# Performance work log

Measured on AMD Instinct MI355X. Metric: run time of the kernel, lower is better.

Reference implementation:

```python
import jax, jax.numpy as jnp
import numpy as np

B, S, D, H = 2, 2048, 2048, 16
HD = D // H  # 128


def setup_inputs() -> dict:
    key = jax.random.key(0)
    ks = jax.random.split(key, 6)
    sc = 0.02
    return {
        "x": jax.random.normal(ks[0], (B, S, D), jnp.float32),
        "attention_mask": jnp.ones((B, S), jnp.int32),
        "w_qkv": jax.random.normal(ks[1], (D, 3 * D), jnp.float32) * sc,
        "b_qkv": jnp.zeros((3 * D,), jnp.float32),
        "w_o": jax.random.normal(ks[2], (D, D), jnp.float32) * sc,
        "b_o": jnp.zeros((D,), jnp.float32),
        "ln1_w": jnp.ones((D,), jnp.float32),
        "w1": jax.random.normal(ks[3], (D, 8 * D), jnp.float32) * sc,
        "b1": jnp.zeros((8 * D,), jnp.float32),
        "w2": jax.random.normal(ks[4], (4 * D, D), jnp.float32) * sc,
        "b2": jnp.zeros((D,), jnp.float32),
        "ln2_w": jnp.ones((D,), jnp.float32),
    }


def rmsnorm(x, w, eps=1e-6):
    rms = jnp.sqrt(jnp.mean(x * x, axis=-1, keepdims=True) + eps)
    return w * (x / rms)


def rope_tables(seq_len, dim, base=10000.0):
    inv_freq = 1.0 / (base ** (jnp.arange(0, dim, 2, dtype=jnp.float32) / dim))
    t = jnp.arange(seq_len, dtype=jnp.float32)
    freqs = t[:, None] * inv_freq[None, :]          # [S, dim/2]
    emb = jnp.concatenate([freqs, freqs], axis=-1)  # [S, dim]
    return jnp.cos(emb), jnp.sin(emb)


def apply_rope(x, cos, sin):
    # Faithful to source: rotate pairs, then out = rot*cos + roll(rot,1)*sin
    xr = x.reshape(*x.shape[:-1], -1, 2)
    x1, x2 = xr[..., 0], xr[..., 1]
    rot = jnp.stack([-x2, x1], axis=-1).reshape(x.shape)
    return rot * cos + jnp.roll(rot, shift=1, axis=-1) * sin


def transformer_layer(x, attention_mask, w_qkv, b_qkv, w_o, b_o, ln1_w, w1, b1, w2, b2, ln2_w):
    residual = x
    qkv = x @ w_qkv + b_qkv                         # [B,S,3D]
    q, k, v = jnp.split(qkv, 3, axis=-1)
    split = lambda t: t.reshape(B, S, H, HD).transpose(0, 2, 1, 3)  # [B,H,S,HD]
    q, k, v = split(q), split(k), split(v)

    cos, sin = rope_tables(S, HD)                   # [S,HD], broadcasts over B,H
    q = apply_rope(q, cos, sin)
    k = apply_rope(k, cos, sin)

    scores = jnp.einsum("bhqd,bhkd->bhqk", q, k) / jnp.sqrt(jnp.float32(HD))
    mask = (attention_mask == 1)[:, None, None, :]  # [B,1,1,S]
    scores = jnp.where(mask, scores, -jnp.inf)
    attn = jax.nn.softmax(scores, axis=-1)
    out = jnp.einsum("bhqk,bhkd->bhqd", attn, v)
    out = out.transpose(0, 2, 1, 3).reshape(B, S, D)
    out = out @ w_o + b_o

    x = rmsnorm(out + residual, ln1_w)
    residual = x
    h = x @ w1 + b1                                 # [B,S,8D]
    h, gate = jnp.split(h, 2, axis=-1)
    h = h * jax.nn.gelu(gate, approximate=False)
    h = h @ w2 + b2
    return rmsnorm(h + residual, ln2_w)


def reference(x, attention_mask, w_qkv, b_qkv, w_o, b_o, ln1_w, w1, b1, w2, b2, ln2_w):
    return transformer_layer(x, attention_mask, w_qkv, b_qkv, w_o, b_o, ln1_w, w1, b1, w2, b2, ln2_w)
```

## Files before the change

### kernel.cpp

```cpp
#include <hip/hip_runtime.h>
#include <cstdint>

typedef unsigned short u16;
typedef __attribute__((ext_vector_type(8))) short short8;
typedef __attribute__((ext_vector_type(8))) unsigned short ushortx8;
typedef __attribute__((ext_vector_type(4))) float floatx4;

#define DEV __device__ __forceinline__

DEV u16 f2bf(float f) {
  union { float f; uint32_t u; } x; x.f = f;
  uint32_t r = x.u + 0x7fffu + ((x.u >> 16) & 1u);
  return (u16)(r >> 16);
}
DEV float bf2f(u16 h) {
  union { float f; uint32_t u; } x; x.u = ((uint32_t)h) << 16;
  return x.f;
}
DEV void gload_lds16(const void* g, void* lds) {
  __builtin_amdgcn_global_load_lds(
      (const __attribute__((address_space(1))) char*)(uintptr_t)g,
      (__attribute__((address_space(3))) char*)(uintptr_t)lds, 16, 0, 0);
}


__global__ __launch_bounds__(256) void k_cvt_bf16(const float* __restrict__ in,
                                                  u16* __restrict__ out, int n) {
  int i = (blockIdx.x * 256 + threadIdx.x) * 4;
  if (i + 3 < n) {
    float4 v = *(const float4*)(in + i);
    ushort4 o;
    o.x = f2bf(v.x); o.y = f2bf(v.y); o.z = f2bf(v.z); o.w = f2bf(v.w);
    *(ushort4*)(out + i) = o;
  }
}

__global__ __launch_bounds__(256) void k_transpose_cvt(const float* __restrict__ W,
                                                       u16* __restrict__ Wt, int R, int C) {
  __shared__ u16 t[32][33];
  int tx = threadIdx.x & 31, ty = threadIdx.x >> 5;
  int r0 = blockIdx.y * 32, c0 = blockIdx.x * 32;
#pragma unroll
  for (int i = ty; i < 32; i += 8)
    t[i][tx] = f2bf(W[(size_t)(r0 + i) * C + c0 + tx]);
  __syncthreads();
#pragma unroll
  for (int i = ty; i < 32; i += 8)
    Wt[(size_t)(c0 + i) * R + r0 + tx] = t[tx][i];
}

__global__ __launch_bounds__(256) void k_rope_tab(float* __restrict__ ct, float* __restrict__ st) {
  int i = blockIdx.x * 256 + threadIdx.x;
  int s = i >> 6, j = i & 63;
  float invf = 1.0f / powf(10000.0f, (float)j * (1.0f / 64.0f));
  float ang = (float)s * invf;
  ct[i] = cosf(ang);
  st[i] = sinf(ang);
}

__global__ __launch_bounds__(256) void k_rope_split(const u16* __restrict__ qkv,
                                                    const float* __restrict__ ct,
                                                    const float* __restrict__ st,
                                                    u16* __restrict__ qr, u16* __restrict__ kr) {
  int bs = blockIdx.x;
  int b = bs >> 11, s = bs & 2047;
  __shared__ float q[2048], k[2048];
  const u16* row = qkv + (size_t)bs * 6144;
  for (int i = threadIdx.x * 4; i < 2048; i += 1024) {
    ushort4 qa = *(const ushort4*)(row + i);
    ushort4 ka = *(const ushort4*)(row + 2048 + i);
    q[i] = bf2f(qa.x); q[i + 1] = bf2f(qa.y); q[i + 2] = bf2f(qa.z); q[i + 3] = bf2f(qa.w);
    k[i] = bf2f(ka.x); k[i + 1] = bf2f(ka.y); k[i + 2] = bf2f(ka.z); k[i + 3] = bf2f(ka.w);
  }
  __syncthreads();
  int i0 = threadIdx.x * 8;
  int h = i0 >> 7, d0 = i0 & 127;
  const float* qh = q + (h << 7);
  const float* kh = k + (h << 7);
  ushortx8 qo, ko;
#pragma unroll
  for (int e = 0; e < 8; ++e) {
    int d = d0 + e;
    int dm1 = (d + 127) & 127;
    float c = ct[(s << 6) + (d & 63)];
    float sn = st[(s << 6) + (d & 63)];
    float rq  = (d & 1)   ? qh[d - 1]   : -qh[d + 1];
    float rq1 = (dm1 & 1) ? qh[dm1 - 1] : -qh[dm1 + 1];
    float rk  = (d & 1)   ? kh[d - 1]   : -kh[d + 1];
    float rk1 = (dm1 & 1) ? kh[dm1 - 1] : -kh[dm1 + 1];
    qo[e] = f2bf(rq * c + rq1 * sn);
    ko[e] = f2bf(rk * c + rk1 * sn);
  }
  size_t obase = (((size_t)b * 16 + h) * 2048 + s) * 128 + d0;
  *(ushortx8*)(qr + obase) = qo;
  *(ushortx8*)(kr + obase) = ko;
}

__global__ __launch_bounds__(256) void k_v_transpose(const u16* __restrict__ qkv,
                                                     u16* __restrict__ vt) {
  __shared__ u16 t[32][33];
  int tx = threadIdx.x & 31, ty = threadIdx.x >> 5;
  int s0 = blockIdx.x * 32;
  int dm0 = (blockIdx.y & 63) * 32;
  int b = blockIdx.y >> 6;
#pragma unroll
  for (int i = ty; i < 32; i += 8)
    t[i][tx] = qkv[((size_t)(b * 2048) + s0 + i) * 6144 + 4096 + dm0 + tx];
  __syncthreads();
#pragma unroll
  for (int i = ty; i < 32; i += 8)
    vt[((size_t)b * 2048 + dm0 + i) * 2048 + s0 + tx] = t[tx][i];
}

template <int EPI>
__global__ __launch_bounds__(512, 2) void k_gemm256(const u16* __restrict__ A,
                                                    const u16* __restrict__ Bt,
                                                    void* __restrict__ C,
                                                    const float* __restrict__ bias,
                                                    int M, int N, int K, int nsplit) {
  __shared__ __align__(16) u16 lds[4][2][8192];
  const int tid = threadIdx.x;
  const int w = tid >> 6, lane = tid & 63;
  const int l15 = lane & 15, l4 = lane >> 4;
  const int wm = w >> 2, wn = w & 3;
  const int nbn = N >> 8;

  const int nwg = gridDim.x;
  const int q = nwg >> 3, r8 = nwg & 7;
  const int xcd = blockIdx.x & 7, loc = blockIdx.x >> 3;
  const int swz = (xcd < r8 ? xcd * (q + 1) : r8 * (q + 1) + (xcd - r8) * q) + loc;
  const int ntiles = nwg / nsplit;
  const int split = swz / ntiles, tix = swz % ntiles;
  const int bm = tix / nbn, bn = tix % nbn;
  const int klen = K / nsplit;
  const int kofs = split * klen;

  const size_t abase = (size_t)bm * 256 * K + kofs;
  const size_t bbase = (size_t)bn * 256 * K + kofs;
  const int nt = klen >> 5;

  const int sr = tid >> 2;
  const int sc = (tid & 3) ^ ((sr >> 1) & 3);
  auto stage = [&](int kt, int li, int op) {
    const u16* src = op ? (Bt + bbase) : (A + abase);
    gload_lds16(src + (size_t)(li * 128 + sr) * K + kt * 32 + sc * 8,
                (void*)&lds[kt & 3][op][(li * 512 + w * 64) * 8]);
  };

  const int fro = l15 * 32 + (l4 ^ ((l15 >> 1) & 3)) * 8;

  floatx4 acc[8][4];
  floatx4 zero = {0.f, 0.f, 0.f, 0.f};
#pragma unroll
  for (int m = 0; m < 8; ++m)
#pragma unroll
    for (int n = 0; n < 4; ++n) acc[m][n] = zero;

  for (int kt = 0; kt < 3; ++kt)
    if (kt < nt) {
      stage(kt, 0, 0); stage(kt, 0, 1);
      stage(kt, 1, 0); stage(kt, 1, 1);
    }

  for (int t = 0; t < nt; ++t) {
    const int buf = t & 3;
    if (t < nt - 2)       asm volatile("s_waitcnt vmcnt(8)" ::: "memory");
    else if (t == nt - 2) asm volatile("s_waitcnt vmcnt(4)" ::: "memory");
    else                  asm volatile("s_waitcnt vmcnt(0)" ::: "memory");
    __builtin_amdgcn_s_barrier();
    asm volatile("" ::: "memory");
    if (t + 3 < nt) {
      stage(t + 3, 0, 0); stage(t + 3, 0, 1);
      stage(t + 3, 1, 0); stage(t + 3, 1, 1);
    }
    const u16* Ab = &lds[buf][0][wm * 4096 + fro];
    const u16* Bb = &lds[buf][1][wn * 2048 + fro];
    short8 av[8], bv[4];
#pragma unroll
    for (int n = 0; n < 4; ++n) bv[n] = *(const short8*)(Bb + n * 512);
#pragma unroll
    for (int i = 0; i < 8; ++i) av[i] = *(const short8*)(Ab + i * 512);
#pragma unroll
    for (int i = 0; i < 8; ++i)
#pragma unroll
      for (int n = 0; n < 4; ++n)
        acc[i][n] = __builtin_amdgcn_mfma_f32_16x16x32_bf16(av[i], bv[n], acc[i][n], 0, 0, 0);
    asm volatile("s_waitcnt lgkmcnt(0)" ::: "memory");
  }

  const int row0 = bm * 256 + wm * 128, col0 = bn * 256 + wn * 64;
  if (EPI == 2) {
    float* P = (float*)C + (size_t)split * M * N;
#pragma unroll
    for (int n = 0; n < 4; ++n) {
      int col = col0 + n * 16 + l15;
#pragma unroll
      for (int m = 0; m < 8; ++m)
#pragma unroll
        for (int j = 0; j < 4; ++j) {
          int row = row0 + m * 16 + l4 * 4 + j;
          P[(size_t)row * N + col] = acc[m][n][j];
        }
    }
  } else {
    __syncthreads();
    u16* ep = ((u16*)lds) + w * 8192;
#pragma unroll
    for (int n = 0; n < 4; ++n) {
      float bb = bias[col0 + n * 16 + l15];
#pragma unroll
      for (int m = 0; m < 8; ++m)
#pragma unroll
        for (int j = 0; j < 4; ++j)
          ep[(m * 16 + l4 * 4 + j) * 64 + n * 16 + l15] = f2bf(acc[m][n][j] + bb);
    }
    const int rr = lane >> 3, cg = lane & 7;
    u16* Cg = (u16*)C;
#pragma unroll
    for (int pass = 0; pass < 16; ++pass) {
      short8 v = *(const short8*)&ep[(pass * 8 + rr) * 64 + cg * 8];
      size_t grow = row0 + pass * 8 + rr;
      *(short8*)&Cg[grow * N + col0 + cg * 8] = v;
    }
  }
}

__global__ __launch_bounds__(512, 4) void k_attn(const u16* __restrict__ Qr,
                                                 const u16* __restrict__ Kr,
                                                 const u16* __restrict__ Vt,
                                                 const int* __restrict__ mask,
                                                 u16* __restrict__ O) {
  constexpr int S = 2048, HD = 128, H = 16;
  __shared__ __align__(16) u16 Ksh[64 * 128];
  __shared__ __align__(16) u16 Vsh[128 * 64];
  __shared__ __align__(16) u16 Psh[8][16 * 72];
  __shared__ float Msh[2048];

  const int bid = blockIdx.x;
  const int xcd = bid & 7, local = bid >> 3;
  const int bh = xcd * 4 + (local >> 4);
  const int qt = local & 15;
  const int b = bh >> 4, h = bh & 15;
  const int tid = threadIdx.x, wave = tid >> 6, lane = tid & 63;
  const int l15 = lane & 15, l4 = lane >> 4;
  const size_t bhs = (size_t)(b * H + h);
  const u16* Qb = Qr + bhs * S * HD;
  const u16* Kb = Kr + bhs * S * HD;
  const u16* Vb = Vt + bhs * HD * S;

  for (int i = tid; i < 2048; i += 512)
    Msh[i] = (mask[b * S + i] == 1) ? 0.0f : -1e30f;

  const int qrow = qt * 128 + wave * 16 + l15;
  short8 qf[4];
#pragma unroll
  for (int kk = 0; kk < 4; ++kk)
    qf[kk] = *(const short8*)&Qb[(size_t)qrow * HD + kk * 32 + l4 * 8];

  float m_run[4], l_run[4];
  floatx4 o_acc[8];
  floatx4 zero = {0.f, 0.f, 0.f, 0.f};
#pragma unroll
  for (int j = 0; j < 4; ++j) { m_run[j] = -1e30f; l_run[j] = 0.f; }
#pragma unroll
  for (int n = 0; n < 8; ++n) o_acc[n] = zero;

  for (int ktile = 0; ktile < S / 64; ++ktile) {
    __syncthreads();
#pragma unroll
    for (int it = 0; it < 2; ++it) {
      int gi = it * 512 + tid;
      {
        int row = gi >> 4, g = gi & 15;
        int gs = (g & 8) | ((g ^ row) & 7);
        gload_lds16(Kb + (size_t)(ktile * 64 + row) * HD + gs * 8,
                    (char*)&Ksh[it * 4096 + wave * 512]);
      }
      {
        int row = gi >> 3, g = gi & 7;
        int gs = (g ^ row) & 7;
        gload_lds16(Vb + (size_t)row * S + ktile * 64 + gs * 8,
                    (char*)&Vsh[it * 4096 + wave * 512]);
      }
    }
    __syncthreads();

    floatx4 s_acc[4];
#pragma unroll
    for (int nf = 0; nf < 4; ++nf) s_acc[nf] = zero;
#pragma unroll
    for (int kk = 0; kk < 4; ++kk) {
#pragma unroll
      for (int nf = 0; nf < 4; ++nf) {
        int key = nf * 16 + l15;
        int G = kk * 4 + l4;
        int lg = (G & 8) | ((G ^ key) & 7);
        short8 kv = *(const short8*)&Ksh[key * 128 + lg * 8];
        s_acc[nf] = __builtin_amdgcn_mfma_f32_16x16x32_bf16(qf[kk], kv, s_acc[nf], 0, 0, 0);
      }
    }

    const float scale = 0.08838834764831845f;
    float p[4][4];
#pragma unroll
    for (int nf = 0; nf < 4; ++nf) {
      float ma = Msh[ktile * 64 + nf * 16 + l15];
#pragma unroll
      for (int j = 0; j < 4; ++j) p[nf][j] = s_acc[nf][j] * scale + ma;
    }
#pragma unroll
    for (int j = 0; j < 4; ++j) {
      float mx = fmaxf(fmaxf(p[0][j], p[1][j]), fmaxf(p[2][j], p[3][j]));
      mx = fmaxf(mx, __shfl_xor(mx, 1));
      mx = fmaxf(mx, __shfl_xor(mx, 2));
      mx = fmaxf(mx, __shfl_xor(mx, 4));
      mx = fmaxf(mx, __shfl_xor(mx, 8));
      float mnew = fmaxf(m_run[j], mx);
      float corr = __expf(m_run[j] - mnew);
      float ps = 0.f;
#pragma unroll
      for (int nf = 0; nf < 4; ++nf) {
        p[nf][j] = __expf(p[nf][j] - mnew);
        ps += p[nf][j];
      }
      ps += __shfl_xor(ps, 1); ps += __shfl_xor(ps, 2);
      ps += __shfl_xor(ps, 4); ps += __shfl_xor(ps, 8);
      l_run[j] = l_run[j] * corr + ps;
      m_run[j] = mnew;
#pragma unroll
      for (int n = 0; n < 8; ++n) o_acc[n][j] *= corr;
    }

#pragma unroll
    for (int nf = 0; nf < 4; ++nf)
#pragma unroll
      for (int j = 0; j < 4; ++j)
        Psh[wave][(l4 * 4 + j) * 72 + nf * 16 + l15] = f2bf(p[nf][j]);

#pragma unroll
    for (int ks = 0; ks < 2; ++ks) {
      short8 pa = *(const short8*)&Psh[wave][l15 * 72 + ks * 32 + l4 * 8];
#pragma unroll
      for (int nf2 = 0; nf2 < 8; ++nf2) {
        int hd = nf2 * 16 + l15;
        int G = ks * 4 + l4;
        short8 vv = *(const short8*)&Vsh[hd * 64 + ((G ^ hd) & 7) * 8];
        o_acc[nf2] = __builtin_amdgcn_mfma_f32_16x16x32_bf16(pa, vv, o_acc[nf2], 0, 0, 0);
      }
    }
  }

#pragma unroll
  for (int j = 0; j < 4; ++j) {
    float inv = 1.0f / l_run[j];
    int srow = qt * 128 + wave * 16 + l4 * 4 + j;
    size_t orow = ((size_t)b * S + srow) * 2048 + h * 128;
#pragma unroll
    for (int nf2 = 0; nf2 < 8; ++nf2)
      O[orow + nf2 * 16 + l15] = f2bf(o_acc[nf2][j] * inv);
  }
}

template <int OUTMODE>
__global__ __launch_bounds__(256) void k_rms_fuse(const float* __restrict__ p0,
                                                  const float* __restrict__ p1,
                                                  const float* __restrict__ bias,
                                                  const float* __restrict__ resid,
                                                  const float* __restrict__ w,
                                                  u16* __restrict__ ob,
                                                  float* __restrict__ of) {
  int row = blockIdx.x;
  int t = threadIdx.x;
  size_t base = (size_t)row * 2048 + t * 8;
  float4 a0 = *(const float4*)(p0 + base);
  float4 a1 = *(const float4*)(p0 + base + 4);
  float4 b0 = *(const float4*)(p1 + base);
  float4 b1 = *(const float4*)(p1 + base + 4);
  float4 r0 = *(const float4*)(resid + base);
  float4 r1 = *(const float4*)(resid + base + 4);
  float4 c0 = *(const float4*)(bias + t * 8);
  float4 c1 = *(const float4*)(bias + t * 8 + 4);
  float v[8];
  v[0] = a0.x + b0.x + r0.x + c0.x; v[1] = a0.y + b0.y + r0.y + c0.y;
  v[2] = a0.z + b0.z + r0.z + c0.z; v[3] = a0.w + b0.w + r0.w + c0.w;
  v[4] = a1.x + b1.x + r1.x + c1.x; v[5] = a1.y + b1.y + r1.y + c1.y;
  v[6] = a1.z + b1.z + r1.z + c1.z; v[7] = a1.w + b1.w + r1.w + c1.w;
  float ss = 0.f;
#pragma unroll
  for (int e = 0; e < 8; ++e) ss += v[e] * v[e];
#pragma unroll
  for (int d = 1; d < 64; d <<= 1) ss += __shfl_xor(ss, d);
  __shared__ float sred[4];
  if ((t & 63) == 0) sred[t >> 6] = ss;
  __syncthreads();
  float tot = sred[0] + sred[1] + sred[2] + sred[3];
  float scale = rsqrtf(tot * (1.0f / 2048.0f) + 1e-6f);
  const float* wp = w + t * 8;
  float o[8];
#pragma unroll
  for (int e = 0; e < 8; ++e) o[e] = v[e] * wp[e] * scale;
  if (OUTMODE == 1) {
    ushort4 q0, q1;
    q0.x = f2bf(o[0]); q0.y = f2bf(o[1]); q0.z = f2bf(o[2]); q0.w = f2bf(o[3]);
    q1.x = f2bf(o[4]); q1.y = f2bf(o[5]); q1.z = f2bf(o[6]); q1.w = f2bf(o[7]);
    *(ushort4*)(ob + base) = q0;
    *(ushort4*)(ob + base + 4) = q1;
  }
  {
    float4 f0, f1;
    f0.x = o[0]; f0.y = o[1]; f0.z = o[2]; f0.w = o[3];
    f1.x = o[4]; f1.y = o[5]; f1.z = o[6]; f1.w = o[7];
    *(float4*)(of + base) = f0;
    *(float4*)(of + base + 4) = f1;
  }
}

__global__ __launch_bounds__(256) void k_gelu_mul(const u16* __restrict__ h,
                                                  u16* __restrict__ act) {
  int i = blockIdx.x * 256 + threadIdx.x;
  int row = i >> 10, c8 = (i & 1023) << 3;
  const u16* hr = h + (size_t)row * 16384 + c8;
  ushortx8 a = *(const ushortx8*)hr;
  ushortx8 g = *(const ushortx8*)(hr + 8192);
  ushortx8 o;
#pragma unroll
  for (int e = 0; e < 8; ++e) {
    float av = bf2f(a[e]), gv = bf2f(g[e]);
    float ge = 0.5f * gv * (1.0f + erff(gv * 0.7071067811865476f));
    o[e] = f2bf(av * ge);
  }
  *(ushortx8*)(act + (size_t)row * 8192 + c8) = o;
}

extern "C" void kernel_launch(void* const* d_in, const int* in_sizes, int n_in,
                              void* d_out, int out_size, void* d_ws, size_t ws_size,
                              hipStream_t stream) {
  const float* x     = (const float*)d_in[0];
  const int*   amask = (const int*)d_in[1];
  const float* w_qkv = (const float*)d_in[2];
  const float* b_qkv = (const float*)d_in[3];
  const float* w_o   = (const float*)d_in[4];
  const float* b_o   = (const float*)d_in[5];
  const float* ln1_w = (const float*)d_in[6];
  const float* w1    = (const float*)d_in[7];
  const float* b1    = (const float*)d_in[8];
  const float* w2    = (const float*)d_in[9];
  const float* b2    = (const float*)d_in[10];
  const float* ln2_w = (const float*)d_in[11];
  float* out = (float*)d_out;

  char* ws = (char*)d_ws;
  u16*   xb    = (u16*)(ws + 0);
  u16*   wqkvT = (u16*)(ws + 16777216);
  u16*   woT   = (u16*)(ws + 41943040);
  u16*   w1T   = (u16*)(ws + 50331648);
  u16*   w2T   = (u16*)(ws + 117440512);
  float* ctab  = (float*)(ws + 150994944);
  float* stab  = (float*)(ws + 151519232);
  u16*   qkv   = (u16*)(ws + 152043520);
  u16*   qr    = (u16*)(ws + 202375168);
  u16*   kr    = (u16*)(ws + 219152384);
  u16*   vt    = (u16*)(ws + 235929600);
  u16*   aout  = (u16*)(ws + 252706816);
  u16*   x1b   = (u16*)(ws + 303038464);
  float* x1f   = (float*)(ws + 319815680);
  float* p01   = (float*)(ws + 152043520);
  u16*   hbuf  = (u16*)(ws + 152043520);
  u16*   act   = (u16*)(ws + 0);

  k_cvt_bf16<<<8192, 256, 0, stream>>>(x, xb, 4096 * 2048);
  k_transpose_cvt<<<dim3(192, 64), 256, 0, stream>>>(w_qkv, wqkvT, 2048, 6144);
  k_transpose_cvt<<<dim3(64, 64), 256, 0, stream>>>(w_o, woT, 2048, 2048);
  k_transpose_cvt<<<dim3(512, 64), 256, 0, stream>>>(w1, w1T, 2048, 16384);
  k_transpose_cvt<<<dim3(64, 256), 256, 0, stream>>>(w2, w2T, 8192, 2048);
  k_rope_tab<<<512, 256, 0, stream>>>(ctab, stab);

  k_gemm256<0><<<16 * 24, 512, 0, stream>>>(xb, wqkvT, qkv, b_qkv, 4096, 6144, 2048, 1);
  k_rope_split<<<4096, 256, 0, stream>>>(qkv, ctab, stab, qr, kr);
  k_v_transpose<<<dim3(64, 128), 256, 0, stream>>>(qkv, vt);
  k_attn<<<512, 512, 0, stream>>>(qr, kr, vt, amask, aout);

  k_gemm256<2><<<16 * 8 * 2, 512, 0, stream>>>(aout, woT, p01, nullptr, 4096, 2048, 2048, 2);
  k_rms_fuse<1><<<4096, 256, 0, stream>>>(p01, p01 + (size_t)4096 * 2048, b_o, x, ln1_w, x1b, x1f);

  k_gemm256<0><<<16 * 64, 512, 0, stream>>>(x1b, w1T, hbuf, b1, 4096, 16384, 2048, 1);
  k_gelu_mul<<<16384, 256, 0, stream>>>(hbuf, act);

  k_gemm256<2><<<16 * 8 * 2, 512, 0, stream>>>(act, w2T, p01, nullptr, 4096, 2048, 8192, 2);
  k_rms_fuse<2><<<4096, 256, 0, stream>>>(p01, p01 + (size_t)4096 * 2048, b2, x1f, ln2_w, nullptr, out);
}
```

Baseline: 973.7 us.

## Fuse GELU-gate into W1 GEMM epilogue via permuted weights; split MFMA loop

The W1 weight is transposed into a permuted column order so that each 256-column output tile holds matching value and gate columns. This lets the GEMM epilogue compute bias plus exact GELU gating and write the 8192-wide activation directly, removing the 16384-wide intermediate buffer and the separate gelu_mul kernel. The GEMM main loop also now issues LDS reads before the global prefetch, splits the MFMA block into two halves with a partial lgkmcnt wait, and adds sched_barrier and setprio hints to overlap LDS latency with compute. Buffer offsets are reshuffled to avoid aliasing with the new layout.

```diff
diff --git a/kernel.cpp b/kernel.cpp
--- a/kernel.cpp
+++ b/kernel.cpp
@@ -47,6 +47,24 @@
 #pragma unroll
   for (int i = ty; i < 32; i += 8)
     Wt[(size_t)(c0 + i) * R + r0 + tx] = t[tx][i];
+}
+
+__global__ __launch_bounds__(256) void k_transpose_w1p(const float* __restrict__ W,
+                                                       u16* __restrict__ Wt) {
+  __shared__ u16 t[32][33];
+  int tx = threadIdx.x & 31, ty = threadIdx.x >> 5;
+  int r0 = blockIdx.y * 32;
+  int c0 = blockIdx.x * 32;
+  int eta = c0 + tx;
+  int Bq = eta >> 8, i = eta & 255, wn = (i >> 6) & 3, r = i & 63, n = r >> 4, tt = r & 15;
+  int src = Bq * 128 + wn * 32 + (n & 1) * 16 + tt + ((n >= 2) ? 8192 : 0);
+#pragma unroll
+  for (int k = ty; k < 32; k += 8)
+    t[k][tx] = f2bf(W[(size_t)(r0 + k) * 16384 + src]);
+  __syncthreads();
+#pragma unroll
+  for (int i2 = ty; i2 < 32; i2 += 8)
+    Wt[(size_t)(c0 + i2) * 2048 + r0 + tx] = t[tx][i2];
 }
 
 __global__ __launch_bounds__(256) void k_rope_tab(float* __restrict__ ct, float* __restrict__ st) {
@@ -167,25 +185,42 @@
     if (t < nt - 2)       asm volatile("s_waitcnt vmcnt(8)" ::: "memory");
     else if (t == nt - 2) asm volatile("s_waitcnt vmcnt(4)" ::: "memory");
     else                  asm volatile("s_waitcnt vmcnt(0)" ::: "memory");
+    __builtin_amdgcn_sched_barrier(0);
     __builtin_amdgcn_s_barrier();
-    asm volatile("" ::: "memory");
+    __builtin_amdgcn_sched_barrier(0);
+    const u16* Ab = &lds[buf][0][wm * 4096 + fro];
+    const u16* Bb = &lds[buf][1][wn * 2048 + fro];
+    short8 bv[4], av[8];
+#pragma unroll
+    for (int n = 0; n < 4; ++n) bv[n] = *(const short8*)(Bb + n * 512);
+#pragma unroll
+    for (int i = 0; i < 4; ++i) av[i] = *(const short8*)(Ab + i * 512);
+    __builtin_amdgcn_sched_barrier(0);
+#pragma unroll
+    for (int i = 4; i < 8; ++i) av[i] = *(const short8*)(Ab + i * 512);
     if (t + 3 < nt) {
       stage(t + 3, 0, 0); stage(t + 3, 0, 1);
       stage(t + 3, 1, 0); stage(t + 3, 1, 1);
     }
-    const u16* Ab = &lds[buf][0][wm * 4096 + fro];
-    const u16* Bb = &lds[buf][1][wn * 2048 + fro];
-    short8 av[8], bv[4];
-#pragma unroll
-    for (int n = 0; n < 4; ++n) bv[n] = *(const short8*)(Bb + n * 512);
-#pragma unroll
-    for (int i = 0; i < 8; ++i) av[i] = *(const short8*)(Ab + i * 512);
-#pragma unroll
-    for (int i = 0; i < 8; ++i)
+    asm volatile("s_waitcnt lgkmcnt(4)" ::: "memory");
+    __builtin_amdgcn_sched_barrier(0);
+    __builtin_amdgcn_s_setprio(1);
+#pragma unroll
+    for (int i = 0; i < 4; ++i)
 #pragma unroll
       for (int n = 0; n < 4; ++n)
         acc[i][n] = __builtin_amdgcn_mfma_f32_16x16x32_bf16(av[i], bv[n], acc[i][n], 0, 0, 0);
+    __builtin_amdgcn_s_setprio(0);
+    __builtin_amdgcn_sched_barrier(0);
     asm volatile("s_waitcnt lgkmcnt(0)" ::: "memory");
+    __builtin_amdgcn_sched_barrier(0);
+    __builtin_amdgcn_s_setprio(1);
+#pragma unroll
+    for (int i = 4; i < 8; ++i)
+#pragma unroll
+      for (int n = 0; n < 4; ++n)
+        acc[i][n] = __builtin_amdgcn_mfma_f32_16x16x32_bf16(av[i], bv[n], acc[i][n], 0, 0, 0);
+    __builtin_amdgcn_s_setprio(0);
   }
 
   const int row0 = bm * 256 + wm * 128, col0 = bn * 256 + wn * 64;
@@ -201,6 +236,33 @@
           int row = row0 + m * 16 + l4 * 4 + j;
           P[(size_t)row * N + col] = acc[m][n][j];
         }
+    }
+  } else if (EPI == 3) {
+    __syncthreads();
+    u16* ep = ((u16*)lds) + w * 4096;
+    const int colA = bn * 128 + wn * 32;
+#pragma unroll
+    for (int n = 0; n < 2; ++n) {
+      float ba = bias[colA + n * 16 + l15];
+      float bg = bias[8192 + colA + n * 16 + l15];
+#pragma unroll
+      for (int m = 0; m < 8; ++m)
+#pragma unroll
+        for (int j = 0; j < 4; ++j) {
+          float a = acc[m][n][j] + ba;
+          float g = acc[m][n + 2][j] + bg;
+          float ge = 0.5f * g * (1.0f + erff(g * 0.7071067811865476f));
+          ep[(m * 16 + l4 * 4 + j) * 32 + n * 16 + l15] = f2bf(a * ge);
+        }
+    }
+    const int rr = lane >> 2, cg = lane & 3;
+    u16* Cg = (u16*)C;
+    const int Nact = N >> 1;
+#pragma unroll
+    for (int pass = 0; pass < 8; ++pass) {
+      short8 v = *(const short8*)&ep[(pass * 16 + rr) * 32 + cg * 8];
+      size_t grow = row0 + pass * 16 + rr;
+      *(short8*)&Cg[grow * Nact + colA + cg * 8] = v;
     }
   } else {
     __syncthreads();
@@ -415,23 +477,6 @@
   }
 }
 
-__global__ __launch_bounds__(256) void k_gelu_mul(const u16* __restrict__ h,
-                                                  u16* __restrict__ act) {
-  int i = blockIdx.x * 256 + threadIdx.x;
-  int row = i >> 10, c8 = (i & 1023) << 3;
-  const u16* hr = h + (size_t)row * 16384 + c8;
-  ushortx8 a = *(const ushortx8*)hr;
-  ushortx8 g = *(const ushortx8*)(hr + 8192);
-  ushortx8 o;
-#pragma unroll
-  for (int e = 0; e < 8; ++e) {
-    float av = bf2f(a[e]), gv = bf2f(g[e]);
-    float ge = 0.5f * gv * (1.0f + erff(gv * 0.7071067811865476f));
-    o[e] = f2bf(av * ge);
-  }
-  *(ushortx8*)(act + (size_t)row * 8192 + c8) = o;
-}
-
 extern "C" void kernel_launch(void* const* d_in, const int* in_sizes, int n_in,
                               void* d_out, int out_size, void* d_ws, size_t ws_size,
                               hipStream_t stream) {
@@ -453,7 +498,7 @@
   u16*   xb    = (u16*)(ws + 0);
   u16*   wqkvT = (u16*)(ws + 16777216);
   u16*   woT   = (u16*)(ws + 41943040);
-  u16*   w1T   = (u16*)(ws + 50331648);
+  u16*   w1Tp  = (u16*)(ws + 50331648);
   u16*   w2T   = (u16*)(ws + 117440512);
   float* ctab  = (float*)(ws + 150994944);
   float* stab  = (float*)(ws + 151519232);
@@ -464,14 +509,14 @@
   u16*   aout  = (u16*)(ws + 252706816);
   u16*   x1b   = (u16*)(ws + 303038464);
   float* x1f   = (float*)(ws + 319815680);
-  float* p01   = (float*)(ws + 152043520);
-  u16*   hbuf  = (u16*)(ws + 152043520);
-  u16*   act   = (u16*)(ws + 0);
+  float* p01a  = (float*)(ws + 152043520);
+  u16*   act   = (u16*)(ws + 152043520);
+  float* p01b  = (float*)(ws + 219152384);
 
   k_cvt_bf16<<<8192, 256, 0, stream>>>(x, xb, 4096 * 2048);
   k_transpose_cvt<<<dim3(192, 64), 256, 0, stream>>>(w_qkv, wqkvT, 2048, 6144);
   k_transpose_cvt<<<dim3(64, 64), 256, 0, stream>>>(w_o, woT, 2048, 2048);
-  k_transpose_cvt<<<dim3(512, 64), 256, 0, stream>>>(w1, w1T, 2048, 16384);
+  k_transpose_w1p<<<dim3(512, 64), 256, 0, stream>>>(w1, w1Tp);
   k_transpose_cvt<<<dim3(64, 256), 256, 0, stream>>>(w2, w2T, 8192, 2048);
   k_rope_tab<<<512, 256, 0, stream>>>(ctab, stab);
 
@@ -480,12 +525,11 @@
   k_v_transpose<<<dim3(64, 128), 256, 0, stream>>>(qkv, vt);
   k_attn<<<512, 512, 0, stream>>>(qr, kr, vt, amask, aout);
 
-  k_gemm256<2><<<16 * 8 * 2, 512, 0, stream>>>(aout, woT, p01, nullptr, 4096, 2048, 2048, 2);
-  k_rms_fuse<1><<<4096, 256, 0, stream>>>(p01, p01 + (size_t)4096 * 2048, b_o, x, ln1_w, x1b, x1f);
-
-  k_gemm256<0><<<16 * 64, 512, 0, stream>>>(x1b, w1T, hbuf, b1, 4096, 16384, 2048, 1);
-  k_gelu_mul<<<16384, 256, 0, stream>>>(hbuf, act);
-
-  k_gemm256<2><<<16 * 8 * 2, 512, 0, stream>>>(act, w2T, p01, nullptr, 4096, 2048, 8192, 2);
-  k_rms_fuse<2><<<4096, 256, 0, stream>>>(p01, p01 + (size_t)4096 * 2048, b2, x1f, ln2_w, nullptr, out);
-}
+  k_gemm256<2><<<16 * 8 * 2, 512, 0, stream>>>(aout, woT, p01a, nullptr, 4096, 2048, 2048, 2);
+  k_rms_fuse<1><<<4096, 256, 0, stream>>>(p01a, p01a + (size_t)4096 * 2048, b_o, x, ln1_w, x1b, x1f);
+
+  k_gemm256<3><<<16 * 64, 512, 0, stream>>>(x1b, w1Tp, act, b1, 4096, 16384, 2048, 1);
+
+  k_gemm256<2><<<16 * 8 * 2, 512, 0, stream>>>(act, w2T, p01b, nullptr, 4096, 2048, 8192, 2);
+  k_rms_fuse<2><<<4096, 256, 0, stream>>>(p01b, p01b + (size_t)4096 * 2048, b2, x1f, ln2_w, nullptr, out);
+}
```

Measured after the change: 944.7 us. 3.0% less time.
